# Performance work log

Hardware: AMD Instinct MI355X
Metric: run time of the kernel (lower is better)

## Reference

```python
import jax, jax.numpy as jnp
import numpy as np

NEG_INF = -1e9


def setup_inputs() -> dict:
    key = jax.random.key(0)
    ks = jax.random.split(key, 8)
    B, S, D = 8, 2048, 1024
    scale = 1.0 / np.sqrt(D)
    src = jax.random.normal(ks[0], (B, S, D), dtype=jnp.float32)
    pad_len = jax.random.randint(ks[1], (B,), 0, S // 10)
    pos = jnp.arange(S)[None, :]
    src_padding_mask = jnp.where(pos >= (S - pad_len)[:, None], NEG_INF, 0.0).astype(jnp.float32)[:, :, None]
    # causal (subsequent) additive mask [S,S]
    src_subsq_mask = jnp.where(jnp.triu(jnp.ones((S, S), dtype=bool), k=1), NEG_INF, 0.0).astype(jnp.float32)
    Wk = jax.random.normal(ks[2], (D, D), dtype=jnp.float32) * scale
    Wv = jax.random.normal(ks[3], (D, D), dtype=jnp.float32) * scale
    Wq = jax.random.normal(ks[4], (D, D), dtype=jnp.float32) * scale
    bk = jnp.zeros((D,), dtype=jnp.float32)
    bv = jnp.zeros((D,), dtype=jnp.float32)
    bq = jnp.zeros((D,), dtype=jnp.float32)
    return {"src": src, "src_padding_mask": src_padding_mask, "src_subsq_mask": src_subsq_mask,
            "Wk": Wk, "bk": bk, "Wv": Wv, "bv": bv, "Wq": Wq, "bq": bq}


def reference(src, src_padding_mask, src_subsq_mask, Wk, bk, Wv, bv, Wq, bq):
    d_model = src.shape[-1]
    # torch nn.Linear: x @ W.T + b
    keys = jnp.einsum('bsd,ed->bse', src, Wk) + bk
    values = jnp.einsum('bsd,ed->bse', src, Wv) + bv
    queries = jnp.einsum('bsd,ed->bse', src, Wq) + bq
    sqrt_d = jnp.asarray(d_model, src.dtype) ** 0.5
    att = jnp.einsum('bqd,bkd->bqk', queries, keys) / sqrt_d   # [B,S,S]
    att = att + jnp.swapaxes(src_padding_mask, 1, 2)           # [B,1,S] broadcast
    att = att + src_subsq_mask[None, :, :]                      # [1,S,S] broadcast
    att_softmax = jax.nn.softmax(att, axis=2)
    att_out = jnp.einsum('bqk,bkd->bqd', att_softmax, values)
    return att_out
```

## Files before the change

kernel.cpp:

```cpp
#include <hip/hip_runtime.h>
#include <cstdint>
#include <cstddef>

#define BATCH 8
#define SEQ   2048
#define DM    1024

typedef _Float16 half8 __attribute__((ext_vector_type(8)));
typedef _Float16 half4v __attribute__((ext_vector_type(4)));
typedef float floatx4 __attribute__((ext_vector_type(4)));
typedef float float4v __attribute__((ext_vector_type(4)));

#define GLOBAL_AS __attribute__((address_space(1)))
#define LDS_AS    __attribute__((address_space(3)))

__device__ __forceinline__ void gl_lds16(const _Float16* g, _Float16* l) {
    __builtin_amdgcn_global_load_lds((const GLOBAL_AS void*)g, (LDS_AS void*)l, 16, 0, 0);
}

__device__ __forceinline__ void gemm_bt_tile(
    const _Float16* __restrict__ A, const _Float16* __restrict__ B,
    int lda, int ldb, int kmax,
    _Float16* As, _Float16* Bs, floatx4 (&acc)[4][4])
{
    const int t = threadIdx.x;
    const int wave = t >> 6, lane = t & 63;
    const int l15 = lane & 15, kq = lane >> 4;
    const int wm = (wave >> 1) * 64, wn = (wave & 1) * 64;
    const int sr = t >> 2;
    const int scc = ((t & 3) ^ ((sr >> 1) & 3)) * 8;
    const int slot = (kq ^ ((l15 >> 1) & 3)) * 8;
    _Float16* AsW = As + wave * 512;
    _Float16* BsW = Bs + wave * 512;

    for (int k0 = 0; k0 < kmax; k0 += 32) {
        __syncthreads();
        gl_lds16(A + (size_t)sr * lda + k0 + scc,        AsW);
        gl_lds16(A + (size_t)(sr + 64) * lda + k0 + scc, AsW + 2048);
        gl_lds16(B + (size_t)sr * ldb + k0 + scc,        BsW);
        gl_lds16(B + (size_t)(sr + 64) * ldb + k0 + scc, BsW + 2048);
        __syncthreads();

        half8 af[4], bfr[4];
        #pragma unroll
        for (int i = 0; i < 4; i++)
            af[i] = *(const half8*)&As[(wm + i * 16 + l15) * 32 + slot];
        #pragma unroll
        for (int j = 0; j < 4; j++)
            bfr[j] = *(const half8*)&Bs[(wn + j * 16 + l15) * 32 + slot];
        #pragma unroll
        for (int i = 0; i < 4; i++)
            #pragma unroll
            for (int j = 0; j < 4; j++)
                acc[i][j] = __builtin_amdgcn_mfma_f32_16x16x32_f16(af[i], bfr[j], acc[i][j], 0, 0, 0);
    }
}

__global__ __launch_bounds__(256) void convert_inputs(
    const float* __restrict__ src,
    const float* __restrict__ Wk, const float* __restrict__ Wv, const float* __restrict__ Wq,
    _Float16* __restrict__ Xh, _Float16* __restrict__ Wh)
{
    const int gid = blockIdx.x * 256 + threadIdx.x;
    const int gs  = gridDim.x * 256;
    const int nX4 = BATCH * SEQ * DM / 4;
    const int nW4 = DM * DM / 4;
    const float4v* s4  = (const float4v*)src;
    const float4v* wk4 = (const float4v*)Wk;
    const float4v* wv4 = (const float4v*)Wv;
    const float4v* wq4 = (const float4v*)Wq;
    half4v* x4 = (half4v*)Xh;
    half4v* w4 = (half4v*)Wh;
    for (int i = gid; i < nX4; i += gs) {
        float4v v = s4[i];
        half4v h;
        #pragma unroll
        for (int e = 0; e < 4; e++) h[e] = (_Float16)v[e];
        x4[i] = h;
    }
    for (int i = gid; i < nW4; i += gs) {
        float4v a = wk4[i], b = wv4[i], c = wq4[i];
        half4v ha, hb, hc;
        #pragma unroll
        for (int e = 0; e < 4; e++) { ha[e] = (_Float16)a[e]; hb[e] = (_Float16)b[e]; hc[e] = (_Float16)c[e]; }
        w4[i]           = ha;
        w4[nW4 + i]     = hb;
        w4[2 * nW4 + i] = hc;
    }
}

__global__ __launch_bounds__(256) void qkv_gemm(
    const _Float16* __restrict__ Xh, const _Float16* __restrict__ Wh,
    const float* __restrict__ bk, const float* __restrict__ bv, const float* __restrict__ bq,
    _Float16* __restrict__ Kh, _Float16* __restrict__ Vt, _Float16* __restrict__ Qh)
{
    __shared__ __align__(16) _Float16 As[128 * 32];
    __shared__ __align__(16) _Float16 Bs[128 * 32];
    const int L = blockIdx.x;
    const int x = L & 7, s = L >> 3;
    const int z = s % 3;
    const int u = s / 3;
    const int by = x * 16 + (u >> 3);
    const int bx = u & 7;

    const _Float16 *A, *B;
    if (z == 1) {
        A = Wh + (size_t)DM * DM + (size_t)bx * 128 * DM;
        B = Xh + (size_t)by * 128 * DM;
    } else {
        A = Xh + (size_t)by * 128 * DM;
        B = Wh + (z == 0 ? (size_t)0 : (size_t)2 * DM * DM) + (size_t)bx * 128 * DM;
    }
    floatx4 acc[4][4] = {};
    gemm_bt_tile(A, B, DM, DM, DM, As, Bs, acc);

    const int lane = threadIdx.x & 63, wave = threadIdx.x >> 6;
    const int l15 = lane & 15, kq = lane >> 4;
    const int wm = (wave >> 1) * 64, wn = (wave & 1) * 64;
    if (z == 1) {
        const int b = by >> 4, st = by & 15;
        #pragma unroll
        for (int i = 0; i < 4; i++)
            #pragma unroll
            for (int j = 0; j < 4; j++)
                #pragma unroll
                for (int rr = 0; rr < 4; rr++) {
                    int d = bx * 128 + wm + i * 16 + kq * 4 + rr;
                    int sIdx = st * 128 + wn + j * 16 + l15;
                    Vt[((size_t)b * DM + d) * SEQ + sIdx] = (_Float16)(acc[i][j][rr] + bv[d]);
                }
    } else {
        const float* bias = (z == 0) ? bk : bq;
        _Float16* outp    = (z == 0) ? Kh : Qh;
        #pragma unroll
        for (int i = 0; i < 4; i++)
            #pragma unroll
            for (int j = 0; j < 4; j++)
                #pragma unroll
                for (int rr = 0; rr < 4; rr++) {
                    int row = by * 128 + wm + i * 16 + kq * 4 + rr;
                    int col = bx * 128 + wn + j * 16 + l15;
                    outp[(size_t)row * DM + col] = (_Float16)(acc[i][j][rr] + bias[col]);
                }
    }
}

__global__ __launch_bounds__(256) void scores_gemm(
    const _Float16* __restrict__ Qh, const _Float16* __restrict__ Kh,
    const float* __restrict__ pad, _Float16* __restrict__ Sc)
{
    __shared__ __align__(16) _Float16 As[128 * 32];
    __shared__ __align__(16) _Float16 Bs[128 * 32];
    const int L = blockIdx.x;
    const int x = L & 7, s = L >> 3;
    const int b = s / 17, w = s % 17;
    int by, bx;
    if (w < 16 - x) { by = 15 - x; bx = w; }
    else            { by = x;      bx = w - (16 - x); }

    const _Float16* A = Qh + ((size_t)b * SEQ + by * 128) * DM;
    const _Float16* B = Kh + ((size_t)b * SEQ + bx * 128) * DM;
    floatx4 acc[4][4] = {};
    gemm_bt_tile(A, B, DM, DM, DM, As, Bs, acc);

    const int lane = threadIdx.x & 63, wave = threadIdx.x >> 6;
    const int l15 = lane & 15, kq = lane >> 4;
    const int wm = (wave >> 1) * 64, wn = (wave & 1) * 64;
    #pragma unroll
    for (int i = 0; i < 4; i++)
        #pragma unroll
        for (int j = 0; j < 4; j++)
            #pragma unroll
            for (int r = 0; r < 4; r++) {
                int row = by * 128 + wm + i * 16 + kq * 4 + r;
                int col = bx * 128 + wn + j * 16 + l15;
                Sc[((size_t)b * SEQ + row) * SEQ + col] =
                    (_Float16)(acc[i][j][r] * 0.03125f + pad[b * SEQ + col]);
            }
}

__global__ __launch_bounds__(256) void softmax_rows(_Float16* __restrict__ Sc)
{
    const int bid = blockIdx.x;
    const int b = bid >> 11, q = bid & (SEQ - 1);
    _Float16* row = Sc + ((size_t)b * SEQ + q) * SEQ;
    const int t = threadIdx.x;
    const int c0 = t * 8;
    __shared__ float red[4];

    half8 v = *(const half8*)(row + c0);
    float f[8];
    float m = -3.0e38f;
    #pragma unroll
    for (int e = 0; e < 8; e++) {
        f[e] = (c0 + e <= q) ? (float)v[e] : -3.0e38f;
        m = fmaxf(m, f[e]);
    }
    #pragma unroll
    for (int o = 32; o > 0; o >>= 1) m = fmaxf(m, __shfl_down(m, o));
    if ((t & 63) == 0) red[t >> 6] = m;
    __syncthreads();
    m = fmaxf(fmaxf(red[0], red[1]), fmaxf(red[2], red[3]));

    float ex[8], s = 0.f;
    #pragma unroll
    for (int e = 0; e < 8; e++) {
        ex[e] = (c0 + e <= q) ? __expf(f[e] - m) : 0.f;
        s += ex[e];
    }
    #pragma unroll
    for (int o = 32; o > 0; o >>= 1) s += __shfl_down(s, o);
    __syncthreads();
    if ((t & 63) == 0) red[t >> 6] = s;
    __syncthreads();
    s = red[0] + red[1] + red[2] + red[3];

    const float inv = 1.0f / s;
    half8 o8;
    #pragma unroll
    for (int e = 0; e < 8; e++) o8[e] = (_Float16)(ex[e] * inv);
    *(half8*)(row + c0) = o8;
}

__global__ __launch_bounds__(256) void pv_gemm(
    const _Float16* __restrict__ P, const _Float16* __restrict__ Vt,
    float* __restrict__ out)
{
    __shared__ __align__(16) _Float16 As[128 * 32];
    __shared__ __align__(16) _Float16 Bs[128 * 32];
    const int L = blockIdx.x;
    const int x = L & 7, s = L >> 3;
    const int b = s >> 4;
    const int r = s & 15;
    const int by = (r < 8) ? (15 - x) : x;
    const int bx = r & 7;

    const _Float16* A = P  + ((size_t)b * SEQ + by * 128) * SEQ;
    const _Float16* B = Vt + ((size_t)b * DM  + bx * 128) * SEQ;
    const int kmax = (by + 1) * 128;
    floatx4 acc[4][4] = {};
    gemm_bt_tile(A, B, SEQ, SEQ, kmax, As, Bs, acc);

    const int lane = threadIdx.x & 63, wave = threadIdx.x >> 6;
    const int l15 = lane & 15, kq = lane >> 4;
    const int wm = (wave >> 1) * 64, wn = (wave & 1) * 64;
    #pragma unroll
    for (int i = 0; i < 4; i++)
        #pragma unroll
        for (int j = 0; j < 4; j++)
            #pragma unroll
            for (int rr = 0; rr < 4; rr++) {
                int row = by * 128 + wm + i * 16 + kq * 4 + rr;
                int col = bx * 128 + wn + j * 16 + l15;
                out[((size_t)b * SEQ + row) * DM + col] = acc[i][j][rr];
            }
}

extern "C" void kernel_launch(void* const* d_in, const int* in_sizes, int n_in,
                              void* d_out, int out_size, void* d_ws, size_t ws_size,
                              hipStream_t stream) {
    const float* src = (const float*)d_in[0];
    const float* pad = (const float*)d_in[1];
    const float* Wk = (const float*)d_in[3];
    const float* bk = (const float*)d_in[4];
    const float* Wv = (const float*)d_in[5];
    const float* bv = (const float*)d_in[6];
    const float* Wq = (const float*)d_in[7];
    const float* bq = (const float*)d_in[8];
    float* out = (float*)d_out;

    char* ws = (char*)d_ws;
    _Float16* Wh = (_Float16*)(ws);
    _Float16* Qh = (_Float16*)(ws + 6291456);
    _Float16* Kh = (_Float16*)(ws + 39845888);
    _Float16* Vt = (_Float16*)(ws + 73400320);
    _Float16* Sc = (_Float16*)(ws + 106954752);
    _Float16* Xh = (_Float16*)d_out;

    convert_inputs<<<2048, 256, 0, stream>>>(src, Wk, Wv, Wq, Xh, Wh);
    qkv_gemm<<<3072, 256, 0, stream>>>(Xh, Wh, bk, bv, bq, Kh, Vt, Qh);
    scores_gemm<<<1088, 256, 0, stream>>>(Qh, Kh, pad, Sc);
    softmax_rows<<<BATCH * SEQ, 256, 0, stream>>>(Sc);
    pv_gemm<<<1024, 256, 0, stream>>>(Sc, Vt, out);
}
```

Before: 459.6 us.

## Double K-step per LDS stage, new swizzle, skip masked softmax columns

The shared GEMM tile loop now stages 64 columns of K per barrier pair instead of 32. It uses an 8-way XOR swizzle and a new per-wave row mapping for the LDS loads, which halves the number of barrier synchronisations and doubles LDS use per block. The QKV GEMM block-index decomposition is reordered so that z is the outer index. The softmax kernel skips loading and storing score tiles beyond the causal 128-block boundary, saving memory traffic on the upper triangle.

```diff
diff --git a/kernel.cpp b/kernel.cpp
--- a/kernel.cpp
+++ b/kernel.cpp
@@ -27,32 +27,52 @@
     const int wave = t >> 6, lane = t & 63;
     const int l15 = lane & 15, kq = lane >> 4;
     const int wm = (wave >> 1) * 64, wn = (wave & 1) * 64;
-    const int sr = t >> 2;
-    const int scc = ((t & 3) ^ ((sr >> 1) & 3)) * 8;
-    const int slot = (kq ^ ((l15 >> 1) & 3)) * 8;
+    const int srow = wave * 8 + (lane >> 3);
+    const int schunk = lane & 7;
     _Float16* AsW = As + wave * 512;
     _Float16* BsW = Bs + wave * 512;
-
-    for (int k0 = 0; k0 < kmax; k0 += 32) {
+    const int cslot = ((kq ^ (l15 & 7)) * 8);
+    const int cslot1 = (((4 + kq) ^ (l15 & 7)) * 8);
+
+    for (int k0 = 0; k0 < kmax; k0 += 64) {
         __syncthreads();
-        gl_lds16(A + (size_t)sr * lda + k0 + scc,        AsW);
-        gl_lds16(A + (size_t)(sr + 64) * lda + k0 + scc, AsW + 2048);
-        gl_lds16(B + (size_t)sr * ldb + k0 + scc,        BsW);
-        gl_lds16(B + (size_t)(sr + 64) * ldb + k0 + scc, BsW + 2048);
+        #pragma unroll
+        for (int i = 0; i < 4; i++) {
+            const int r = srow + i * 32;
+            const int gcol = (schunk ^ (r & 7)) * 8;
+            gl_lds16(A + (size_t)r * lda + k0 + gcol, AsW + i * 2048);
+            gl_lds16(B + (size_t)r * ldb + k0 + gcol, BsW + i * 2048);
+        }
         __syncthreads();
 
-        half8 af[4], bfr[4];
-        #pragma unroll
-        for (int i = 0; i < 4; i++)
-            af[i] = *(const half8*)&As[(wm + i * 16 + l15) * 32 + slot];
-        #pragma unroll
-        for (int j = 0; j < 4; j++)
-            bfr[j] = *(const half8*)&Bs[(wn + j * 16 + l15) * 32 + slot];
-        #pragma unroll
-        for (int i = 0; i < 4; i++)
+        {
+            half8 af[4], bfr[4];
+            #pragma unroll
+            for (int i = 0; i < 4; i++)
+                af[i] = *(const half8*)&As[(wm + i * 16 + l15) * 64 + cslot];
             #pragma unroll
             for (int j = 0; j < 4; j++)
-                acc[i][j] = __builtin_amdgcn_mfma_f32_16x16x32_f16(af[i], bfr[j], acc[i][j], 0, 0, 0);
+                bfr[j] = *(const half8*)&Bs[(wn + j * 16 + l15) * 64 + cslot];
+            #pragma unroll
+            for (int i = 0; i < 4; i++)
+                #pragma unroll
+                for (int j = 0; j < 4; j++)
+                    acc[i][j] = __builtin_amdgcn_mfma_f32_16x16x32_f16(af[i], bfr[j], acc[i][j], 0, 0, 0);
+        }
+        {
+            half8 af[4], bfr[4];
+            #pragma unroll
+            for (int i = 0; i < 4; i++)
+                af[i] = *(const half8*)&As[(wm + i * 16 + l15) * 64 + cslot1];
+            #pragma unroll
+            for (int j = 0; j < 4; j++)
+                bfr[j] = *(const half8*)&Bs[(wn + j * 16 + l15) * 64 + cslot1];
+            #pragma unroll
+            for (int i = 0; i < 4; i++)
+                #pragma unroll
+                for (int j = 0; j < 4; j++)
+                    acc[i][j] = __builtin_amdgcn_mfma_f32_16x16x32_f16(af[i], bfr[j], acc[i][j], 0, 0, 0);
+        }
     }
 }
 
@@ -94,14 +114,14 @@
     const float* __restrict__ bk, const float* __restrict__ bv, const float* __restrict__ bq,
     _Float16* __restrict__ Kh, _Float16* __restrict__ Vt, _Float16* __restrict__ Qh)
 {
-    __shared__ __align__(16) _Float16 As[128 * 32];
-    __shared__ __align__(16) _Float16 Bs[128 * 32];
+    __shared__ __align__(16) _Float16 As[128 * 64];
+    __shared__ __align__(16) _Float16 Bs[128 * 64];
     const int L = blockIdx.x;
     const int x = L & 7, s = L >> 3;
-    const int z = s % 3;
-    const int u = s / 3;
-    const int by = x * 16 + (u >> 3);
-    const int bx = u & 7;
+    const int z = s >> 7;
+    const int r = s & 127;
+    const int by = x * 16 + (r >> 3);
+    const int bx = r & 7;
 
     const _Float16 *A, *B;
     if (z == 1) {
@@ -149,8 +169,8 @@
     const _Float16* __restrict__ Qh, const _Float16* __restrict__ Kh,
     const float* __restrict__ pad, _Float16* __restrict__ Sc)
 {
-    __shared__ __align__(16) _Float16 As[128 * 32];
-    __shared__ __align__(16) _Float16 Bs[128 * 32];
+    __shared__ __align__(16) _Float16 As[128 * 64];
+    __shared__ __align__(16) _Float16 Bs[128 * 64];
     const int L = blockIdx.x;
     const int x = L & 7, s = L >> 3;
     const int b = s / 17, w = s % 17;
@@ -184,16 +204,20 @@
     const int bid = blockIdx.x;
     const int b = bid >> 11, q = bid & (SEQ - 1);
     _Float16* row = Sc + ((size_t)b * SEQ + q) * SEQ;
+    const int n = q + 1;
+    const int kmaxr = ((q >> 7) + 1) << 7;
     const int t = threadIdx.x;
     const int c0 = t * 8;
+    const bool active = (c0 < kmaxr);
     __shared__ float red[4];
 
-    half8 v = *(const half8*)(row + c0);
+    half8 v = {};
+    if (active) v = *(const half8*)(row + c0);
     float f[8];
     float m = -3.0e38f;
     #pragma unroll
     for (int e = 0; e < 8; e++) {
-        f[e] = (c0 + e <= q) ? (float)v[e] : -3.0e38f;
+        f[e] = (active && (c0 + e < n)) ? (float)v[e] : -3.0e38f;
         m = fmaxf(m, f[e]);
     }
     #pragma unroll
@@ -205,7 +229,7 @@
     float ex[8], s = 0.f;
     #pragma unroll
     for (int e = 0; e < 8; e++) {
-        ex[e] = (c0 + e <= q) ? __expf(f[e] - m) : 0.f;
+        ex[e] = (f[e] > -1.0e38f) ? __expf(f[e] - m) : 0.f;
         s += ex[e];
     }
     #pragma unroll
@@ -215,19 +239,21 @@
     __syncthreads();
     s = red[0] + red[1] + red[2] + red[3];
 
-    const float inv = 1.0f / s;
-    half8 o8;
-    #pragma unroll
-    for (int e = 0; e < 8; e++) o8[e] = (_Float16)(ex[e] * inv);
-    *(half8*)(row + c0) = o8;
+    if (active) {
+        const float inv = 1.0f / s;
+        half8 o8;
+        #pragma unroll
+        for (int e = 0; e < 8; e++) o8[e] = (_Float16)(ex[e] * inv);
+        *(half8*)(row + c0) = o8;
+    }
 }
 
 __global__ __launch_bounds__(256) void pv_gemm(
     const _Float16* __restrict__ P, const _Float16* __restrict__ Vt,
     float* __restrict__ out)
 {
-    __shared__ __align__(16) _Float16 As[128 * 32];
-    __shared__ __align__(16) _Float16 Bs[128 * 32];
+    __shared__ __align__(16) _Float16 As[128 * 64];
+    __shared__ __align__(16) _Float16 Bs[128 * 64];
     const int L = blockIdx.x;
     const int x = L & 7, s = L >> 3;
     const int b = s >> 4;
```

After: 418.5 us. 1.1x faster.
